# Kernel tuning notes

Hardware: AMD Instinct MI355X
Metric: run time of the kernel (lower is better)

## Reference

```python
import jax, jax.numpy as jnp
import numpy as np

B, TQ, TKV, D, H = 2, 1024, 1024, 1024, 16
HD = D // H
BUCKETS, MAX_REL = 32, 128
SPAN = BUCKETS  # pos_ebd_size


def make_log_bucket_position(rel_pos, bucket_size, max_position):
    sign = jnp.sign(rel_pos)
    mid = bucket_size // 2
    abs_pos = jnp.where((rel_pos < mid) & (rel_pos > -mid), mid - 1, jnp.abs(rel_pos))
    log_pos = jnp.ceil(jnp.log(abs_pos.astype(jnp.float32) / mid)
                       / np.float32(np.log((max_position - 1) / mid)) * (mid - 1)) + mid
    return jnp.where(abs_pos <= mid, rel_pos, (log_pos * sign).astype(rel_pos.dtype))


def setup_inputs():
    key = jax.random.key(0)
    ks = jax.random.split(key, 12)
    s = 0.02
    f32 = jnp.float32
    return {
        "query_states": jax.random.normal(ks[0], (B, TQ, D), f32),
        "key_value_states": jax.random.normal(ks[1], (B, TKV, D), f32),
        "Wq": jax.random.normal(ks[2], (D, D), f32) * s, "bq": jnp.zeros((D,), f32),
        "Wk": jax.random.normal(ks[3], (D, D), f32) * s, "bk": jnp.zeros((D,), f32),
        "Wv": jax.random.normal(ks[4], (D, D), f32) * s, "bv": jnp.zeros((D,), f32),
        "Wo": jax.random.normal(ks[5], (D, D), f32) * s, "bo": jnp.zeros((D,), f32),
        "Wpk": jax.random.normal(ks[6], (D, D), f32) * s, "bpk": jnp.zeros((D,), f32),
        "Wpq": jax.random.normal(ks[7], (D, D), f32) * s, "bpq": jnp.zeros((D,), f32),
        "rel_emb": jax.random.normal(ks[8], (2 * SPAN, D), f32) * s,
        "ln_g": jnp.ones((D,), f32), "ln_b": jnp.zeros((D,), f32),
        "attention_mask": jnp.zeros((B, TKV), jnp.bool_),
    }


def reference(query_states, key_value_states, Wq, bq, Wk, bk, Wv, bv, Wo, bo,
              Wpk, bpk, Wpq, bpq, rel_emb, ln_g, ln_b, attention_mask):
    # projections -> [B,H,T,hd]
    q = (query_states @ Wq.T + bq).reshape(B, TQ, H, HD).transpose(0, 2, 1, 3)
    k = (key_value_states @ Wk.T + bk).reshape(B, TKV, H, HD).transpose(0, 2, 1, 3)
    v = (key_value_states @ Wv.T + bv).reshape(B, TKV, H, HD).transpose(0, 2, 1, 3)
    scale = jnp.sqrt(jnp.float32(HD * 3))  # scale_factor = 1 + c2p + p2c
    scores = jnp.einsum('bhqd,bhkd->bhqk', q, k) / scale

    # layer-normalized relative embeddings [2*SPAN, D]
    mu = rel_emb.mean(-1, keepdims=True)
    var = ((rel_emb - mu) ** 2).mean(-1, keepdims=True)
    re = (rel_emb - mu) * jax.lax.rsqrt(var + 1e-5) * ln_g + ln_b
    pos_k = (re @ Wpk.T + bpk).reshape(2 * SPAN, H, HD).transpose(1, 0, 2)  # [H,2S,hd]
    pos_q = (re @ Wpq.T + bpq).reshape(2 * SPAN, H, HD).transpose(1, 0, 2)

    rel = make_log_bucket_position(jnp.arange(TQ)[:, None] - jnp.arange(TKV)[None, :],
                                   BUCKETS, MAX_REL)                      # [Tq,Tkv]
    c2p_pos = jnp.clip(rel + SPAN, 0, 2 * SPAN - 1)
    p2c_pos = jnp.clip(-rel + SPAN, 0, 2 * SPAN - 1)
    pscale = jnp.sqrt(jnp.float32(HD * 2))

    # c2p: gather along relative-position axis
    c2p = jnp.einsum('bhqd,hpd->bhqp', q, pos_k)                          # [B,H,Tq,2S]
    iq = jnp.arange(TQ)[:, None]
    c2p_g = c2p[:, :, iq, c2p_pos]                                        # [B,H,Tq,Tkv]

    # p2c: gather then transpose (requires Tq == Tkv, as in original torch expand)
    p2c = jnp.einsum('bhkd,hpd->bhkp', k, pos_q)                          # [B,H,Tkv,2S]
    ik = jnp.arange(TKV)[:, None]
    p2c_g = p2c[:, :, ik, p2c_pos].transpose(0, 1, 3, 2)                  # [B,H,Tq,Tkv]

    scores = scores + c2p_g / pscale + p2c_g / pscale
    scores = jnp.where(attention_mask[:, None, None, :], -jnp.inf, scores)
    probs = jax.nn.softmax(scores.astype(jnp.float32), axis=-1).astype(q.dtype)

    ctx = jnp.einsum('bhqk,bhkd->bhqd', probs, v).transpose(0, 2, 1, 3).reshape(B, TQ, D)
    return ctx @ Wo.T + bo
```

## Files before the change

### kernel.cpp

```cpp
#include <hip/hip_runtime.h>
#include <hip/hip_bf16.h>
#include <math.h>

#define B   2
#define TQ  1024
#define TKV 1024
#define D   1024
#define H   16
#define HD  64
#define P   64
#define SPAN 32

#define NEG_INF (-3.0e38f)

typedef __attribute__((ext_vector_type(8))) short bf16x8;
typedef __attribute__((ext_vector_type(4))) float f32x4;
typedef unsigned short ushort_t;

static constexpr size_t RE_OFF   = 0;
static constexpr size_t POSK_OFF = (size_t)64 * 1024;
static constexpr size_t POSQ_OFF = (size_t)128 * 1024;
static constexpr size_t FLOATS_END = (size_t)192 * 1024;
static constexpr size_t SHORT_BASE_BYTES = FLOATS_END * 4;
static constexpr size_t C2P_S  = 0;
static constexpr size_t P2C_S  = (size_t)2 * 1024 * 1024;
static constexpr size_t QH_S   = (size_t)4 * 1024 * 1024;
static constexpr size_t QL_S   = (size_t)6 * 1024 * 1024;
static constexpr size_t KH_S   = (size_t)8 * 1024 * 1024;
static constexpr size_t KL_S   = (size_t)10 * 1024 * 1024;
static constexpr size_t VTH_S  = (size_t)12 * 1024 * 1024;
static constexpr size_t VTL_S  = (size_t)14 * 1024 * 1024;
static constexpr size_t CTXH_S = (size_t)16 * 1024 * 1024;
static constexpr size_t CTXL_S = (size_t)18 * 1024 * 1024;
static constexpr size_t AKVH_S = (size_t)20 * 1024 * 1024;
static constexpr size_t AKVL_S = (size_t)22 * 1024 * 1024;
static constexpr size_t TAB_OFF_BYTES = SHORT_BASE_BYTES + (size_t)24 * 1024 * 1024 * 2;

__device__ __forceinline__ void split2(float x, unsigned short& h, unsigned short& l) {
  unsigned int u = __float_as_uint(x);
  h = (unsigned short)(u >> 16);
  float r = x - __uint_as_float(u & 0xffff0000u);
  unsigned int v = __float_as_uint(r);
  v += 0x7fffu + ((v >> 16) & 1u);
  l = (unsigned short)(v >> 16);
}

__device__ __forceinline__ unsigned short bf16rn(float x) {
  unsigned int v = __float_as_uint(x);
  v += 0x7fffu + ((v >> 16) & 1u);
  return (unsigned short)(v >> 16);
}

__device__ __forceinline__ float bf2f(unsigned short u) {
  return __uint_as_float(((unsigned int)u) << 16);
}

__global__ __launch_bounds__(256) void presplit_kernel(const float* __restrict__ in,
    ushort_t* __restrict__ oh, ushort_t* __restrict__ ol) {
  size_t i = ((size_t)blockIdx.x * 256 + threadIdx.x) * 8;
  float4 a = *(const float4*)&in[i];
  float4 b = *(const float4*)&in[i + 4];
  float xs[8] = {a.x, a.y, a.z, a.w, b.x, b.y, b.z, b.w};
  bf16x8 th, tl;
  #pragma unroll
  for (int j = 0; j < 8; j++) {
    unsigned short hh, ll;
    split2(xs[j], hh, ll);
    th[j] = (short)hh; tl[j] = (short)ll;
  }
  *(bf16x8*)&oh[i] = th;
  *(bf16x8*)&ol[i] = tl;
}

__global__ __launch_bounds__(256) void ln_kernel(const float* __restrict__ x,
    const float* __restrict__ g, const float* __restrict__ bta, float* __restrict__ out) {
  const int row = blockIdx.x;
  const float* xr = x + (size_t)row * D;
  const int tid = threadIdx.x;
  __shared__ float red[4];
  float s = 0.f;
  for (int i = tid; i < D; i += 256) s += xr[i];
  #pragma unroll
  for (int off = 32; off; off >>= 1) s += __shfl_down(s, off);
  if ((tid & 63) == 0) red[tid >> 6] = s;
  __syncthreads();
  float mu = (red[0] + red[1] + red[2] + red[3]) * (1.0f / D);
  __syncthreads();
  float vs = 0.f;
  for (int i = tid; i < D; i += 256) { float dd = xr[i] - mu; vs += dd * dd; }
  #pragma unroll
  for (int off = 32; off; off >>= 1) vs += __shfl_down(vs, off);
  if ((tid & 63) == 0) red[tid >> 6] = vs;
  __syncthreads();
  float var = (red[0] + red[1] + red[2] + red[3]) * (1.0f / D);
  float rs = rsqrtf(var + 1e-5f);
  for (int i = tid; i < D; i += 256)
    out[(size_t)row * D + i] = (xr[i] - mu) * rs * g[i] + bta[i];
}

__global__ void tab_kernel(unsigned char* __restrict__ tab) {
  int i = blockIdx.x * 256 + threadIdx.x;
  if (i >= 2047) return;
  int d = i - 1023;
  int ad = d < 0 ? -d : d;
  int bucket;
  if (ad <= 16) {
    bucket = d;
  } else {
    double x = log((double)ad / 16.0) / log(127.0 / 16.0) * 15.0;
    double xr = floor(x + 0.5);
    double xc = (fabs(x - xr) < 1e-9) ? xr : ceil(x);
    int li = (int)xc + 16;
    bucket = (d > 0) ? li : -li;
  }
  int t = bucket + SPAN;
  t = t < 0 ? 0 : (t > 63 ? 63 : t);
  tab[i] = (unsigned char)t;
}

__global__ __launch_bounds__(256) void gemm_pos(const float* __restrict__ A,
    const float* __restrict__ W0, const float* __restrict__ b0, float* __restrict__ C0,
    const float* __restrict__ W1, const float* __restrict__ b1, float* __restrict__ C1) {
  const float* W = blockIdx.z ? W1 : W0;
  const float* bias = blockIdx.z ? b1 : b0;
  float* C = blockIdx.z ? C1 : C0;

  __shared__ short sAh[64 * 32], sAl[64 * 32], sBh[64 * 32], sBl[64 * 32];
  const int t = threadIdx.x;
  const int bn = blockIdx.x * 64;
  const int wid = t >> 6, lane = t & 63;
  const int wr = wid >> 1, wc = wid & 1;
  const int fr = lane & 15, fo = (lane >> 4) * 8;
  const int srow = t >> 3, scol = (t & 7) * 4;

  f32x4 acc[2][2];
  #pragma unroll
  for (int i = 0; i < 2; i++)
    #pragma unroll
    for (int j = 0; j < 2; j++) acc[i][j] = (f32x4){0.f, 0.f, 0.f, 0.f};

  float4 rA[2], rW[2];
  auto ld = [&](int k0) {
    #pragma unroll
    for (int i = 0; i < 2; i++) {
      rA[i] = *(const float4*)&A[(size_t)(srow + 32 * i) * 1024 + k0 + scol];
      rW[i] = *(const float4*)&W[(size_t)(bn + srow + 32 * i) * 1024 + k0 + scol];
    }
  };
  ld(0);

  for (int k0 = 0; k0 < 1024; k0 += 32) {
    __syncthreads();
    #pragma unroll
    for (int i = 0; i < 2; i++) {
      int row = srow + 32 * i;
      unsigned short h0,h1,h2,h3,l0,l1,l2,l3;
      split2(rA[i].x,h0,l0); split2(rA[i].y,h1,l1); split2(rA[i].z,h2,l2); split2(rA[i].w,h3,l3);
      *(short4*)&sAh[row * 32 + scol] = make_short4((short)h0,(short)h1,(short)h2,(short)h3);
      *(short4*)&sAl[row * 32 + scol] = make_short4((short)l0,(short)l1,(short)l2,(short)l3);
      split2(rW[i].x,h0,l0); split2(rW[i].y,h1,l1); split2(rW[i].z,h2,l2); split2(rW[i].w,h3,l3);
      *(short4*)&sBh[row * 32 + scol] = make_short4((short)h0,(short)h1,(short)h2,(short)h3);
      *(short4*)&sBl[row * 32 + scol] = make_short4((short)l0,(short)l1,(short)l2,(short)l3);
    }
    if (k0 + 32 < 1024) ld(k0 + 32);
    __syncthreads();

    bf16x8 ah[2], al[2], bh[2], bl[2];
    #pragma unroll
    for (int mf = 0; mf < 2; mf++) {
      int r = (wr * 32 + mf * 16 + fr) * 32 + fo;
      ah[mf] = *(const bf16x8*)&sAh[r];
      al[mf] = *(const bf16x8*)&sAl[r];
    }
    #pragma unroll
    for (int nf = 0; nf < 2; nf++) {
      int r = (wc * 32 + nf * 16 + fr) * 32 + fo;
      bh[nf] = *(const bf16x8*)&sBh[r];
      bl[nf] = *(const bf16x8*)&sBl[r];
    }
    #pragma unroll
    for (int mf = 0; mf < 2; mf++)
      #pragma unroll
      for (int nf = 0; nf < 2; nf++) {
        acc[mf][nf] = __builtin_amdgcn_mfma_f32_16x16x32_bf16(ah[mf], bh[nf], acc[mf][nf], 0, 0, 0);
        acc[mf][nf] = __builtin_amdgcn_mfma_f32_16x16x32_bf16(ah[mf], bl[nf], acc[mf][nf], 0, 0, 0);
        acc[mf][nf] = __builtin_amdgcn_mfma_f32_16x16x32_bf16(al[mf], bh[nf], acc[mf][nf], 0, 0, 0);
      }
  }

  #pragma unroll
  for (int mf = 0; mf < 2; mf++) {
    int rbase = wr * 32 + mf * 16 + (lane >> 4) * 4;
    #pragma unroll
    for (int nf = 0; nf < 2; nf++) {
      int col = bn + wc * 32 + nf * 16 + fr;
      float bb = bias[col];
      #pragma unroll
      for (int r = 0; r < 4; r++)
        C[(size_t)(rbase + r) * 1024 + col] = acc[mf][nf][r] + bb;
    }
  }
}

__global__ __launch_bounds__(256) void gemm_split(
    const float* __restrict__ Aq,
    const ushort_t* __restrict__ AKVH, const ushort_t* __restrict__ AKVL,
    const float* __restrict__ W0, const float* __restrict__ W1, const float* __restrict__ W2,
    const float* __restrict__ b0, const float* __restrict__ b1, const float* __restrict__ b2,
    ushort_t* __restrict__ QH_, ushort_t* __restrict__ QL_,
    ushort_t* __restrict__ KH_, ushort_t* __restrict__ KL_,
    ushort_t* __restrict__ VH_, ushort_t* __restrict__ VL_,
    int K) {
  const int z = blockIdx.z;
  const float* W = (z == 0) ? W0 : (z == 1) ? W1 : W2;
  const float* bias = (z == 0) ? b0 : (z == 1) ? b1 : b2;

  const int flat2 = blockIdx.y * 16 + blockIdx.x;
  const int nid = (flat2 & 7) * 32 + (flat2 >> 3);
  const int bn = (nid & 15) * 64;
  const int bm = (nid >> 4) * 128;

  __shared__ short sAhi[128 * 32];
  __shared__ short sAlo[128 * 32];
  __shared__ short sBhi[64 * 32];
  __shared__ short sBlo[64 * 32];

  const int t = threadIdx.x;
  const int wid = t >> 6, lane = t & 63;
  const int wr = wid >> 1, wc = wid & 1;
  const int fr = lane & 15, fo = (lane >> 4) * 8;

  f32x4 acc[4][2];
  #pragma unroll
  for (int i = 0; i < 4; i++)
    #pragma unroll
    for (int j = 0; j < 2; j++)
      acc[i][j] = (f32x4){0.f, 0.f, 0.f, 0.f};

  const int srow = t >> 3;
  const int scol = (t & 7) * 4;
  const int ar = t >> 1;
  const int ac = (t & 1) * 16;

  float4 rA[4], rW[2];
  bf16x8 rAH[2], rAL[2];
  auto ld = [&](int k0) {
    if (z == 0) {
      #pragma unroll
      for (int i = 0; i < 4; i++)
        rA[i] = *(const float4*)&Aq[(size_t)(bm + srow + 32 * i) * K + k0 + scol];
    } else {
      const size_t abase = (size_t)(bm + ar) * K + k0 + ac;
      rAH[0] = *(const bf16x8*)&AKVH[abase];
      rAH[1] = *(const bf16x8*)&AKVH[abase + 8];
      rAL[0] = *(const bf16x8*)&AKVL[abase];
      rAL[1] = *(const bf16x8*)&AKVL[abase + 8];
    }
    #pragma unroll
    for (int i = 0; i < 2; i++)
      rW[i] = *(const float4*)&W[(size_t)(bn + srow + 32 * i) * K + k0 + scol];
  };
  ld(0);

  for (int k0 = 0; k0 < K; k0 += 32) {
    __syncthreads();
    if (z == 0) {
      #pragma unroll
      for (int i = 0; i < 4; i++) {
        int row = srow + 32 * i;
        unsigned short h0, h1, h2, h3, l0, l1, l2, l3;
        split2(rA[i].x, h0, l0); split2(rA[i].y, h1, l1); split2(rA[i].z, h2, l2); split2(rA[i].w, h3, l3);
        *(short4*)&sAhi[row * 32 + scol] = make_short4((short)h0, (short)h1, (short)h2, (short)h3);
        *(short4*)&sAlo[row * 32 + scol] = make_short4((short)l0, (short)l1, (short)l2, (short)l3);
      }
    } else {
      *(bf16x8*)&sAhi[ar * 32 + ac]     = rAH[0];
      *(bf16x8*)&sAhi[ar * 32 + ac + 8] = rAH[1];
      *(bf16x8*)&sAlo[ar * 32 + ac]     = rAL[0];
      *(bf16x8*)&sAlo[ar * 32 + ac + 8] = rAL[1];
    }
    #pragma unroll
    for (int i = 0; i < 2; i++) {
      int row = srow + 32 * i;
      unsigned short h0, h1, h2, h3, l0, l1, l2, l3;
      split2(rW[i].x, h0, l0); split2(rW[i].y, h1, l1); split2(rW[i].z, h2, l2); split2(rW[i].w, h3, l3);
      *(short4*)&sBhi[row * 32 + scol] = make_short4((short)h0, (short)h1, (short)h2, (short)h3);
      *(short4*)&sBlo[row * 32 + scol] = make_short4((short)l0, (short)l1, (short)l2, (short)l3);
    }
    if (k0 + 32 < K) ld(k0 + 32);
    __syncthreads();

    bf16x8 ah[4], al[4], bh[2], bl[2];
    #pragma unroll
    for (int mf = 0; mf < 4; mf++) {
      int r = (wr * 64 + mf * 16 + fr) * 32 + fo;
      ah[mf] = *(const bf16x8*)&sAhi[r];
      al[mf] = *(const bf16x8*)&sAlo[r];
    }
    #pragma unroll
    for (int nf = 0; nf < 2; nf++) {
      int r = (wc * 32 + nf * 16 + fr) * 32 + fo;
      bh[nf] = *(const bf16x8*)&sBhi[r];
      bl[nf] = *(const bf16x8*)&sBlo[r];
    }
    #pragma unroll
    for (int mf = 0; mf < 4; mf++)
      #pragma unroll
      for (int nf = 0; nf < 2; nf++) {
        acc[mf][nf] = __builtin_amdgcn_mfma_f32_16x16x32_bf16(ah[mf], bh[nf], acc[mf][nf], 0, 0, 0);
        acc[mf][nf] = __builtin_amdgcn_mfma_f32_16x16x32_bf16(ah[mf], bl[nf], acc[mf][nf], 0, 0, 0);
        acc[mf][nf] = __builtin_amdgcn_mfma_f32_16x16x32_bf16(al[mf], bh[nf], acc[mf][nf], 0, 0, 0);
      }
  }

  if (z == 2) {
    #pragma unroll
    for (int mf = 0; mf < 4; mf++) {
      int m0 = bm + wr * 64 + mf * 16 + (lane >> 4) * 4;
      int bb2 = m0 >> 10, t0 = m0 & 1023;
      #pragma unroll
      for (int nf = 0; nf < 2; nf++) {
        int col = bn + wc * 32 + nf * 16 + fr;
        int hh = col >> 6, dd = col & 63;
        float bvv = bias[col];
        unsigned short h4[4], l4[4];
        #pragma unroll
        for (int r = 0; r < 4; r++) split2(acc[mf][nf][r] + bvv, h4[r], l4[r]);
        size_t dst = (((size_t)bb2 * 16 + hh) * 64 + dd) * 1024 + t0;
        *(short4*)&VH_[dst] = make_short4((short)h4[0], (short)h4[1], (short)h4[2], (short)h4[3]);
        *(short4*)&VL_[dst] = make_short4((short)l4[0], (short)l4[1], (short)l4[2], (short)l4[3]);
      }
    }
  } else {
    ushort_t* OH = (z == 0) ? QH_ : KH_;
    ushort_t* OL = (z == 0) ? QL_ : KL_;
    #pragma unroll
    for (int mf = 0; mf < 4; mf++) {
      int rbase = bm + wr * 64 + mf * 16 + (lane >> 4) * 4;
      #pragma unroll
      for (int nf = 0; nf < 2; nf++) {
        int col = bn + wc * 32 + nf * 16 + fr;
        float bb = bias[col];
        #pragma unroll
        for (int r = 0; r < 4; r++) {
          unsigned short hh, ll;
          split2(acc[mf][nf][r] + bb, hh, ll);
          OH[(size_t)(rbase + r) * 1024 + col] = hh;
          OL[(size_t)(rbase + r) * 1024 + col] = ll;
        }
      }
    }
  }
}

__global__ __launch_bounds__(256) void gemm_out(
    const ushort_t* __restrict__ AH, const ushort_t* __restrict__ AL,
    const float* __restrict__ W, const float* __restrict__ bias, float* __restrict__ C) {
  __shared__ short sAh[64 * 32], sAl[64 * 32], sBh[64 * 32], sBl[64 * 32];
  const int t = threadIdx.x;
  const int flat2 = blockIdx.y * 16 + blockIdx.x;
  const int nid = (flat2 & 7) * 64 + (flat2 >> 3);
  const int bn = (nid & 15) * 64;
  const int bm = (nid >> 4) * 64;
  const int wid = t >> 6, lane = t & 63;
  const int wr = wid >> 1, wc = wid & 1;
  const int fr = lane & 15, fo = (lane >> 4) * 8;
  const int arow = t >> 2, achk = (t & 3) * 8;
  const int srow = t >> 3, scol = (t & 7) * 4;

  f32x4 acc[2][2];
  #pragma unroll
  for (int i = 0; i < 2; i++)
    #pragma unroll
    for (int j = 0; j < 2; j++) acc[i][j] = (f32x4){0.f, 0.f, 0.f, 0.f};

  bf16x8 rAH, rAL;
  float4 rW[2];
  auto ld = [&](int k0) {
    rAH = *(const bf16x8*)&AH[(size_t)(bm + arow) * 1024 + k0 + achk];
    rAL = *(const bf16x8*)&AL[(size_t)(bm + arow) * 1024 + k0 + achk];
    #pragma unroll
    for (int i = 0; i < 2; i++)
      rW[i] = *(const float4*)&W[(size_t)(bn + srow + 32 * i) * 1024 + k0 + scol];
  };
  ld(0);

  for (int k0 = 0; k0 < 1024; k0 += 32) {
    __syncthreads();
    *(bf16x8*)&sAh[arow * 32 + achk] = rAH;
    *(bf16x8*)&sAl[arow * 32 + achk] = rAL;
    #pragma unroll
    for (int i = 0; i < 2; i++) {
      int row = srow + 32 * i;
      unsigned short h0,h1,h2,h3,l0,l1,l2,l3;
      split2(rW[i].x,h0,l0); split2(rW[i].y,h1,l1); split2(rW[i].z,h2,l2); split2(rW[i].w,h3,l3);
      *(short4*)&sBh[row * 32 + scol] = make_short4((short)h0,(short)h1,(short)h2,(short)h3);
      *(short4*)&sBl[row * 32 + scol] = make_short4((short)l0,(short)l1,(short)l2,(short)l3);
    }
    if (k0 + 32 < 1024) ld(k0 + 32);
    __syncthreads();

    bf16x8 ah[2], al[2], bh[2], bl[2];
    #pragma unroll
    for (int mf = 0; mf < 2; mf++) {
      int r = (wr * 32 + mf * 16 + fr) * 32 + fo;
      ah[mf] = *(const bf16x8*)&sAh[r];
      al[mf] = *(const bf16x8*)&sAl[r];
    }
    #pragma unroll
    for (int nf = 0; nf < 2; nf++) {
      int r = (wc * 32 + nf * 16 + fr) * 32 + fo;
      bh[nf] = *(const bf16x8*)&sBh[r];
      bl[nf] = *(const bf16x8*)&sBl[r];
    }
    #pragma unroll
    for (int mf = 0; mf < 2; mf++)
      #pragma unroll
      for (int nf = 0; nf < 2; nf++) {
        acc[mf][nf] = __builtin_amdgcn_mfma_f32_16x16x32_bf16(ah[mf], bh[nf], acc[mf][nf], 0, 0, 0);
        acc[mf][nf] = __builtin_amdgcn_mfma_f32_16x16x32_bf16(ah[mf], bl[nf], acc[mf][nf], 0, 0, 0);
        acc[mf][nf] = __builtin_amdgcn_mfma_f32_16x16x32_bf16(al[mf], bh[nf], acc[mf][nf], 0, 0, 0);
      }
  }

  #pragma unroll
  for (int mf = 0; mf < 2; mf++) {
    int rbase = bm + wr * 32 + mf * 16 + (lane >> 4) * 4;
    #pragma unroll
    for (int nf = 0; nf < 2; nf++) {
      int col = bn + wc * 32 + nf * 16 + fr;
      float bb = bias[col];
      #pragma unroll
      for (int r = 0; r < 4; r++)
        C[(size_t)(rbase + r) * 1024 + col] = acc[mf][nf][r] + bb;
    }
  }
}

__global__ __launch_bounds__(256) void relproj_kernel(
    const ushort_t* __restrict__ XH0, const ushort_t* __restrict__ XL0,
    const float* __restrict__ P0, ushort_t* __restrict__ O0,
    const ushort_t* __restrict__ XH1, const ushort_t* __restrict__ XL1,
    const float* __restrict__ P1, ushort_t* __restrict__ O1) {
  const int z = blockIdx.z;
  const ushort_t* XH = z ? XH1 : XH0;
  const ushort_t* XL = z ? XL1 : XL0;
  const float* POS = z ? P1 : P0;
  ushort_t* out = z ? O1 : O0;
  const int bh = blockIdx.y, b = bh >> 4, h = bh & 15;
  const int t0 = blockIdx.x * 64;
  __shared__ __align__(16) float sx[64][68];
  __shared__ __align__(16) float sp[64][68];
  const int tid = threadIdx.x;
  for (int i = tid; i < 4096; i += 256) {
    int r = i >> 6, d = i & 63;
    size_t idx = ((size_t)b * TQ + t0 + r) * D + h * HD + d;
    sx[d][r] = bf2f(XH[idx]) + bf2f(XL[idx]);
    sp[d][r] = POS[(size_t)r * D + h * HD + d];
  }
  __syncthreads();
  const int tx = tid & 15, ty = tid >> 4;
  float acc[4][4] = {};
  for (int d = 0; d < 64; d++) {
    float4 a4 = *(const float4*)&sx[d][ty * 4];
    float4 b4 = *(const float4*)&sp[d][tx * 4];
    float av[4] = {a4.x, a4.y, a4.z, a4.w};
    float bv[4] = {b4.x, b4.y, b4.z, b4.w};
    #pragma unroll
    for (int i = 0; i < 4; i++)
      #pragma unroll
      for (int j = 0; j < 4; j++)
        acc[i][j] += av[i] * bv[j];
  }
  const float inv_ps = 0.08838834764831845f;
  #pragma unroll
  for (int i = 0; i < 4; i++)
    #pragma unroll
    for (int j = 0; j < 4; j++)
      out[((size_t)bh * TQ + t0 + ty * 4 + i) * P + tx * 4 + j] = bf16rn(acc[i][j] * inv_ps);
}

__global__ __launch_bounds__(256) void attn_mfma(
    const ushort_t* __restrict__ QHB, const ushort_t* __restrict__ QLB,
    const ushort_t* __restrict__ KH, const ushort_t* __restrict__ KL,
    const ushort_t* __restrict__ VTH, const ushort_t* __restrict__ VTL,
    const ushort_t* __restrict__ c2p, const ushort_t* __restrict__ p2c,
    const unsigned char* __restrict__ mask, const unsigned char* __restrict__ tab,
    ushort_t* __restrict__ CTXH, ushort_t* __restrict__ CTXL) {
  const int flat = blockIdx.y * gridDim.x + blockIdx.x;
  const int nid = (flat & 7) * 64 + (flat >> 3);
  const int bh = nid >> 4, b = bh >> 4, h = bh & 15;
  const int q0 = (nid & 15) * 64;

  const int tid = threadIdx.x;
  const int wid = tid >> 6, lane = tid & 63;
  const int g = lane >> 4, fr = lane & 15;

  __shared__ __align__(16) short sKh[4096], sKl[4096], sVh[4096], sVl[4096];
  __shared__ __align__(16) ushort_t sc2p[64][72];
  __shared__ __align__(16) ushort_t sp2c[64][72];
  __shared__ unsigned char stab[2048];
  __shared__ unsigned char smask[64];

  bf16x8 qh[2], ql[2];
  {
    const int qrow = q0 + wid * 16 + fr;
    const size_t qidx = ((size_t)b * TQ + qrow) * D + h * HD + g * 8;
    #pragma unroll
    for (int ks = 0; ks < 2; ks++) {
      qh[ks] = *(const bf16x8*)&QHB[qidx + ks * 32];
      ql[ks] = *(const bf16x8*)&QLB[qidx + ks * 32];
    }
  }

  const int sr = tid >> 2;
  const int sj0 = tid & 3;
  const int smf = sr >> 4, sfr = sr & 15;
  const int cb = (tid & 3) * 16;
  const int qloc = wid * 16 + fr;

  {
    const ushort_t* cp = c2p + ((size_t)bh * TQ + q0 + sr) * P + cb;
    *(bf16x8*)&sc2p[sr][cb]     = *(const bf16x8*)cp;
    *(bf16x8*)&sc2p[sr][cb + 8] = *(const bf16x8*)(cp + 8);
  }
  for (int i = tid; i < 2047; i += 256) stab[i] = tab[i];
  __syncthreads();
  const float c2p0  = bf2f(sc2p[qloc][0]);
  const float c2p63 = bf2f(sc2p[qloc][63]);

  f32x4 acc[4];
  #pragma unroll
  for (int nf = 0; nf < 4; nf++) acc[nf] = (f32x4){0.f, 0.f, 0.f, 0.f};
  float m_run = NEG_INF, l_run = 0.f;

  const float inv_s = 0.07216878364870323f;

  bf16x8 rKh[2], rKl[2], rVh[2], rVl[2], rP0, rP1;
  unsigned char rmask = 0;

  auto load_tile = [&](int kt) {
    const int k0n = kt * 64;
    const size_t kbase = ((size_t)b * TKV + k0n + sr) * D + h * HD;
    const size_t vbase = ((size_t)bh * HD + sr) * TKV + k0n;
    const ushort_t* pp = p2c + ((size_t)bh * TKV + k0n + sr) * P + cb;
    #pragma unroll
    for (int u = 0; u < 2; u++) {
      int jj = sj0 + u * 4;
      rKh[u] = *(const bf16x8*)(KH + kbase + jj * 8);
      rKl[u] = *(const bf16x8*)(KL + kbase + jj * 8);
      rVh[u] = *(const bf16x8*)(VTH + vbase + jj * 8);
      rVl[u] = *(const bf16x8*)(VTL + vbase + jj * 8);
    }
    rP0 = *(const bf16x8*)pp;
    rP1 = *(const bf16x8*)(pp + 8);
    if (tid < 64) rmask = mask[(size_t)b * TKV + k0n + tid];
  };

  load_tile(0);

  for (int kt = 0; kt < TKV / 64; kt++) {
    const int k0 = kt * 64;
    __syncthreads();
    #pragma unroll
    for (int u = 0; u < 2; u++) {
      int jj = sj0 + u * 4;
      int sub = smf * 8 + (jj >> 2) * 4 + (jj & 3);
      *(bf16x8*)&sKh[sub * 128 + sfr * 8] = rKh[u];
      *(bf16x8*)&sKl[sub * 128 + sfr * 8] = rKl[u];
      *(bf16x8*)&sVh[sub * 128 + sfr * 8] = rVh[u];
      *(bf16x8*)&sVl[sub * 128 + sfr * 8] = rVl[u];
    }
    *(bf16x8*)&sp2c[sr][cb]     = rP0;
    *(bf16x8*)&sp2c[sr][cb + 8] = rP1;
    if (tid < 64) smask[tid] = rmask;
    if (kt + 1 < TKV / 64) load_tile(kt + 1);
    __syncthreads();

    f32x4 st[4];
    #pragma unroll
    for (int mf = 0; mf < 4; mf++) st[mf] = (f32x4){0.f, 0.f, 0.f, 0.f};
    __builtin_amdgcn_s_setprio(1);
    #pragma unroll
    for (int mf = 0; mf < 4; mf++) {
      #pragma unroll
      for (int ks = 0; ks < 2; ks++) {
        bf16x8 kh = *(const bf16x8*)&sKh[(mf * 8 + ks * 4 + g) * 128 + fr * 8];
        bf16x8 kl = *(const bf16x8*)&sKl[(mf * 8 + ks * 4 + g) * 128 + fr * 8];
        st[mf] = __builtin_amdgcn_mfma_f32_16x16x32_bf16(kh, qh[ks], st[mf], 0, 0, 0);
        st[mf] = __builtin_amdgcn_mfma_f32_16x16x32_bf16(kh, ql[ks], st[mf], 0, 0, 0);
        st[mf] = __builtin_amdgcn_mfma_f32_16x16x32_bf16(kl, qh[ks], st[mf], 0, 0, 0);
      }
    }
    __builtin_amdgcn_s_setprio(0);

    const int dtile = q0 - k0;
    float pv[4][4];
    float lmax = NEG_INF;
    if (dtile >= 192 || dtile <= -192) {
      const int C = (dtile >= 192) ? 63 : 0;
      const float cbias = (dtile >= 192) ? c2p63 : c2p0;
      #pragma unroll
      for (int mf = 0; mf < 4; mf++) {
        #pragma unroll
        for (int rr = 0; rr < 4; rr++) {
          int kj = mf * 16 + g * 4 + rr;
          float v = st[mf][rr] * inv_s + (cbias + bf2f(sp2c[kj][C]));
          v = smask[kj] ? NEG_INF : v;
          pv[mf][rr] = v;
          lmax = fmaxf(lmax, v);
        }
      }
    } else {
      const int dq = q0 + qloc - k0 + 1023;
      const ushort_t* c2prow = &sc2p[qloc][0];
      #pragma unroll
      for (int mf = 0; mf < 4; mf++) {
        #pragma unroll
        for (int rr = 0; rr < 4; rr++) {
          int kj = mf * 16 + g * 4 + rr;
          int tbi = stab[dq - kj];
          float v = st[mf][rr] * inv_s + (bf2f(c2prow[tbi]) + bf2f(sp2c[kj][tbi]));
          v = smask[kj] ? NEG_INF : v;
          pv[mf][rr] = v;
          lmax = fmaxf(lmax, v);
        }
      }
    }
    lmax = fmaxf(lmax, __shfl_xor(lmax, 16));
    lmax = fmaxf(lmax, __shfl_xor(lmax, 32));
    if (!__all(lmax <= m_run)) {
      float mnew = fmaxf(m_run, lmax);
      float fac = __expf(m_run - mnew);
      m_run = mnew;
      l_run *= fac;
      float facr[4];
      #pragma unroll
      for (int rr = 0; rr < 4; rr++) facr[rr] = __shfl(fac, g * 4 + rr);
      #pragma unroll
      for (int nf = 0; nf < 4; nf++)
        #pragma unroll
        for (int rr = 0; rr < 4; rr++) acc[nf][rr] *= facr[rr];
    }
    float psum = 0.f;
    #pragma unroll
    for (int mf = 0; mf < 4; mf++)
      #pragma unroll
      for (int rr = 0; rr < 4; rr++) {
        float e = __expf(pv[mf][rr] - m_run);
        pv[mf][rr] = e;
        psum += e;
      }
    psum += __shfl_xor(psum, 16);
    psum += __shfl_xor(psum, 32);
    l_run += psum;

    bf16x8 pa[2];
    #pragma unroll
    for (int ks = 0; ks < 2; ks++) {
      bf16x8 t;
      #pragma unroll
      for (int j = 0; j < 8; j++) {
        int src = ((2 * (g & 1) + (j >> 2)) << 4) | fr;
        float v0 = __shfl(pv[2 * ks][j & 3], src);
        float v1 = __shfl(pv[2 * ks + 1][j & 3], src);
        float pvv = (g >> 1) ? v1 : v0;
        t[j] = (short)bf16rn(pvv);
      }
      pa[ks] = t;
    }

    __builtin_amdgcn_s_setprio(1);
    #pragma unroll
    for (int nf = 0; nf < 4; nf++) {
      #pragma unroll
      for (int ks = 0; ks < 2; ks++) {
        bf16x8 vh = *(const bf16x8*)&sVh[(nf * 8 + ks * 4 + g) * 128 + fr * 8];
        bf16x8 vl = *(const bf16x8*)&sVl[(nf * 8 + ks * 4 + g) * 128 + fr * 8];
        acc[nf] = __builtin_amdgcn_mfma_f32_16x16x32_bf16(pa[ks], vh, acc[nf], 0, 0, 0);
        acc[nf] = __builtin_amdgcn_mfma_f32_16x16x32_bf16(pa[ks], vl, acc[nf], 0, 0, 0);
      }
    }
    __builtin_amdgcn_s_setprio(0);
  }

  float invl[4];
  #pragma unroll
  for (int rr = 0; rr < 4; rr++) invl[rr] = 1.0f / __shfl(l_run, g * 4 + rr);
  #pragma unroll
  for (int nf = 0; nf < 4; nf++) {
    #pragma unroll
    for (int rr = 0; rr < 4; rr++) {
      int qrow = q0 + wid * 16 + g * 4 + rr;
      int dcol = h * HD + nf * 16 + fr;
      size_t idx = ((size_t)b * TQ + qrow) * D + dcol;
      unsigned short hh, ll;
      split2(acc[nf][rr] * invl[rr], hh, ll);
      CTXH[idx] = hh;
      CTXL[idx] = ll;
    }
  }
}

extern "C" void kernel_launch(void* const* d_in, const int* in_sizes, int n_in,
                              void* d_out, int out_size, void* d_ws, size_t ws_size,
                              hipStream_t stream) {
  const float* query = (const float*)d_in[0];
  const float* kv    = (const float*)d_in[1];
  const float* Wq  = (const float*)d_in[2];   const float* bq  = (const float*)d_in[3];
  const float* Wk  = (const float*)d_in[4];   const float* bk  = (const float*)d_in[5];
  const float* Wv  = (const float*)d_in[6];   const float* bv  = (const float*)d_in[7];
  const float* Wo  = (const float*)d_in[8];   const float* bo  = (const float*)d_in[9];
  const float* Wpk = (const float*)d_in[10];  const float* bpk = (const float*)d_in[11];
  const float* Wpq = (const float*)d_in[12];  const float* bpq = (const float*)d_in[13];
  const float* rel_emb = (const float*)d_in[14];
  const float* ln_g = (const float*)d_in[15];
  const float* ln_b = (const float*)d_in[16];
  const unsigned char* amask = (const unsigned char*)d_in[17];

  float* ws = (float*)d_ws;
  float* rebuf   = ws + RE_OFF;
  float* poskbuf = ws + POSK_OFF;
  float* posqbuf = ws + POSQ_OFF;
  ushort_t* sbase = (ushort_t*)((char*)d_ws + SHORT_BASE_BYTES);
  ushort_t* c2pbuf = sbase + C2P_S;
  ushort_t* p2cbuf = sbase + P2C_S;
  ushort_t* QH   = sbase + QH_S;
  ushort_t* QL   = sbase + QL_S;
  ushort_t* KH   = sbase + KH_S;
  ushort_t* KL   = sbase + KL_S;
  ushort_t* VTH  = sbase + VTH_S;
  ushort_t* VTL  = sbase + VTL_S;
  ushort_t* CTXH = sbase + CTXH_S;
  ushort_t* CTXL = sbase + CTXL_S;
  ushort_t* AKVH = sbase + AKVH_S;
  ushort_t* AKVL = sbase + AKVL_S;
  unsigned char* tab = (unsigned char*)d_ws + TAB_OFF_BYTES;

  ln_kernel<<<64, 256, 0, stream>>>(rel_emb, ln_g, ln_b, rebuf);
  tab_kernel<<<8, 256, 0, stream>>>(tab);
  presplit_kernel<<<1024, 256, 0, stream>>>(kv, AKVH, AKVL);
  gemm_pos<<<dim3(16, 1, 2), 256, 0, stream>>>(rebuf, Wpk, bpk, poskbuf, Wpq, bpq, posqbuf);
  gemm_split<<<dim3(16, 16, 3), 256, 0, stream>>>(
      query, AKVH, AKVL,  Wq, Wk, Wv,  bq, bk, bv,
      QH, QL, KH, KL, VTH, VTL, 1024);
  relproj_kernel<<<dim3(16, 32, 2), 256, 0, stream>>>(
      QH, QL, poskbuf, c2pbuf, KH, KL, posqbuf, p2cbuf);
  attn_mfma<<<dim3(16, 32), 256, 0, stream>>>(QH, QL, KH, KL, VTH, VTL,
                                              c2pbuf, p2cbuf, amask, tab, CTXH, CTXL);
  gemm_out<<<dim3(16, 32), 256, 0, stream>>>(CTXH, CTXL, Wo, bo, (float*)d_out);
}
```

Before: 199.4 us.

## Fuse preprocessing kernels, remap GEMM tile order, and move relproj to MFMA

Three small prep kernels (kv bf16 split, rel_emb layernorm, bucket table) are merged into one launch to cut launch overhead. The block-to-tile mapping in gemm_split and gemm_out is changed so that blocks sharing one XCD (flat2&7) cover a compact 2D region for better L2 reuse. The scalar-FMA relative-position projection is replaced by a split-bf16 MFMA kernel (hi/lo three-product emulation) with larger per-block tiles. This keeps near-fp32 accuracy but gives fewer blocks in relproj, and the fused kernel has branch-divergent block roles.

```diff
diff --git a/kernel.cpp b/kernel.cpp
--- a/kernel.cpp
+++ b/kernel.cpp
@@ -55,67 +55,68 @@
   return __uint_as_float(((unsigned int)u) << 16);
 }
 
-__global__ __launch_bounds__(256) void presplit_kernel(const float* __restrict__ in,
-    ushort_t* __restrict__ oh, ushort_t* __restrict__ ol) {
-  size_t i = ((size_t)blockIdx.x * 256 + threadIdx.x) * 8;
-  float4 a = *(const float4*)&in[i];
-  float4 b = *(const float4*)&in[i + 4];
-  float xs[8] = {a.x, a.y, a.z, a.w, b.x, b.y, b.z, b.w};
-  bf16x8 th, tl;
-  #pragma unroll
-  for (int j = 0; j < 8; j++) {
-    unsigned short hh, ll;
-    split2(xs[j], hh, ll);
-    th[j] = (short)hh; tl[j] = (short)ll;
-  }
-  *(bf16x8*)&oh[i] = th;
-  *(bf16x8*)&ol[i] = tl;
-}
-
-__global__ __launch_bounds__(256) void ln_kernel(const float* __restrict__ x,
-    const float* __restrict__ g, const float* __restrict__ bta, float* __restrict__ out) {
-  const int row = blockIdx.x;
-  const float* xr = x + (size_t)row * D;
+__global__ __launch_bounds__(256) void fused_pre(const float* __restrict__ kv,
+    ushort_t* __restrict__ oh, ushort_t* __restrict__ ol,
+    const float* __restrict__ re_in, const float* __restrict__ ln_g,
+    const float* __restrict__ ln_b, float* __restrict__ re_out,
+    unsigned char* __restrict__ tab) {
+  const int bid = blockIdx.x;
   const int tid = threadIdx.x;
-  __shared__ float red[4];
-  float s = 0.f;
-  for (int i = tid; i < D; i += 256) s += xr[i];
-  #pragma unroll
-  for (int off = 32; off; off >>= 1) s += __shfl_down(s, off);
-  if ((tid & 63) == 0) red[tid >> 6] = s;
-  __syncthreads();
-  float mu = (red[0] + red[1] + red[2] + red[3]) * (1.0f / D);
-  __syncthreads();
-  float vs = 0.f;
-  for (int i = tid; i < D; i += 256) { float dd = xr[i] - mu; vs += dd * dd; }
-  #pragma unroll
-  for (int off = 32; off; off >>= 1) vs += __shfl_down(vs, off);
-  if ((tid & 63) == 0) red[tid >> 6] = vs;
-  __syncthreads();
-  float var = (red[0] + red[1] + red[2] + red[3]) * (1.0f / D);
-  float rs = rsqrtf(var + 1e-5f);
-  for (int i = tid; i < D; i += 256)
-    out[(size_t)row * D + i] = (xr[i] - mu) * rs * g[i] + bta[i];
-}
-
-__global__ void tab_kernel(unsigned char* __restrict__ tab) {
-  int i = blockIdx.x * 256 + threadIdx.x;
-  if (i >= 2047) return;
-  int d = i - 1023;
-  int ad = d < 0 ? -d : d;
-  int bucket;
-  if (ad <= 16) {
-    bucket = d;
+  if (bid < 1024) {
+    size_t i = ((size_t)bid * 256 + tid) * 8;
+    float4 a = *(const float4*)&kv[i];
+    float4 b = *(const float4*)&kv[i + 4];
+    float xs[8] = {a.x, a.y, a.z, a.w, b.x, b.y, b.z, b.w};
+    bf16x8 th, tl;
+    #pragma unroll
+    for (int j = 0; j < 8; j++) {
+      unsigned short hh, ll;
+      split2(xs[j], hh, ll);
+      th[j] = (short)hh; tl[j] = (short)ll;
+    }
+    *(bf16x8*)&oh[i] = th;
+    *(bf16x8*)&ol[i] = tl;
+  } else if (bid < 1088) {
+    const int row = bid - 1024;
+    const float* xr = re_in + (size_t)row * D;
+    __shared__ float red[4];
+    float s = 0.f;
+    for (int i = tid; i < D; i += 256) s += xr[i];
+    #pragma unroll
+    for (int off = 32; off; off >>= 1) s += __shfl_down(s, off);
+    if ((tid & 63) == 0) red[tid >> 6] = s;
+    __syncthreads();
+    float mu = (red[0] + red[1] + red[2] + red[3]) * (1.0f / D);
+    __syncthreads();
+    float vs = 0.f;
+    for (int i = tid; i < D; i += 256) { float dd = xr[i] - mu; vs += dd * dd; }
+    #pragma unroll
+    for (int off = 32; off; off >>= 1) vs += __shfl_down(vs, off);
+    if ((tid & 63) == 0) red[tid >> 6] = vs;
+    __syncthreads();
+    float var = (red[0] + red[1] + red[2] + red[3]) * (1.0f / D);
+    float rs = rsqrtf(var + 1e-5f);
+    for (int i = tid; i < D; i += 256)
+      re_out[(size_t)row * D + i] = (xr[i] - mu) * rs * ln_g[i] + ln_b[i];
   } else {
-    double x = log((double)ad / 16.0) / log(127.0 / 16.0) * 15.0;
-    double xr = floor(x + 0.5);
-    double xc = (fabs(x - xr) < 1e-9) ? xr : ceil(x);
-    int li = (int)xc + 16;
-    bucket = (d > 0) ? li : -li;
-  }
-  int t = bucket + SPAN;
-  t = t < 0 ? 0 : (t > 63 ? 63 : t);
-  tab[i] = (unsigned char)t;
+    int i = (bid - 1088) * 256 + tid;
+    if (i >= 2047) return;
+    int d = i - 1023;
+    int ad = d < 0 ? -d : d;
+    int bucket;
+    if (ad <= 16) {
+      bucket = d;
+    } else {
+      double x = log((double)ad / 16.0) / log(127.0 / 16.0) * 15.0;
+      double xr = floor(x + 0.5);
+      double xc = (fabs(x - xr) < 1e-9) ? xr : ceil(x);
+      int li = (int)xc + 16;
+      bucket = (d > 0) ? li : -li;
+    }
+    int t = bucket + SPAN;
+    t = t < 0 ? 0 : (t > 63 ? 63 : t);
+    tab[i] = (unsigned char)t;
+  }
 }
 
 __global__ __launch_bounds__(256) void gemm_pos(const float* __restrict__ A,
@@ -216,9 +217,9 @@
   const float* bias = (z == 0) ? b0 : (z == 1) ? b1 : b2;
 
   const int flat2 = blockIdx.y * 16 + blockIdx.x;
-  const int nid = (flat2 & 7) * 32 + (flat2 >> 3);
-  const int bn = (nid & 15) * 64;
-  const int bm = (nid >> 4) * 128;
+  const int x = flat2 & 7, w = flat2 >> 3;
+  const int bm = ((x >> 1) * 4 + (w >> 3)) * 128;
+  const int bn = ((x & 1) * 8 + (w & 7)) * 64;
 
   __shared__ short sAhi[128 * 32];
   __shared__ short sAlo[128 * 32];
@@ -359,9 +360,9 @@
   __shared__ short sAh[64 * 32], sAl[64 * 32], sBh[64 * 32], sBl[64 * 32];
   const int t = threadIdx.x;
   const int flat2 = blockIdx.y * 16 + blockIdx.x;
-  const int nid = (flat2 & 7) * 64 + (flat2 >> 3);
-  const int bn = (nid & 15) * 64;
-  const int bm = (nid >> 4) * 64;
+  const int x = flat2 & 7, w = flat2 >> 3;
+  const int bm = ((x >> 1) * 8 + (w >> 3)) * 64;
+  const int bn = ((x & 1) * 8 + (w & 7)) * 64;
   const int wid = t >> 6, lane = t & 63;
   const int wr = wid >> 1, wc = wid & 1;
   const int fr = lane & 15, fo = (lane >> 4) * 8;
@@ -437,47 +438,86 @@
   }
 }
 
-__global__ __launch_bounds__(256) void relproj_kernel(
-    const ushort_t* __restrict__ XH0, const ushort_t* __restrict__ XL0,
-    const float* __restrict__ P0, ushort_t* __restrict__ O0,
-    const ushort_t* __restrict__ XH1, const ushort_t* __restrict__ XL1,
-    const float* __restrict__ P1, ushort_t* __restrict__ O1) {
+__global__ __launch_bounds__(256) void relproj_mfma(
+    const ushort_t* __restrict__ QH, const ushort_t* __restrict__ QL,
+    const ushort_t* __restrict__ KH, const ushort_t* __restrict__ KL,
+    const float* __restrict__ POSK, const float* __restrict__ POSQ,
+    ushort_t* __restrict__ O0, ushort_t* __restrict__ O1) {
   const int z = blockIdx.z;
-  const ushort_t* XH = z ? XH1 : XH0;
-  const ushort_t* XL = z ? XL1 : XL0;
-  const float* POS = z ? P1 : P0;
+  const ushort_t* XH = z ? KH : QH;
+  const ushort_t* XL = z ? KL : QL;
+  const float* POS = z ? POSQ : POSK;
   ushort_t* out = z ? O1 : O0;
   const int bh = blockIdx.y, b = bh >> 4, h = bh & 15;
-  const int t0 = blockIdx.x * 64;
-  __shared__ __align__(16) float sx[64][68];
-  __shared__ __align__(16) float sp[64][68];
+  const int t0 = blockIdx.x * 256;
+
   const int tid = threadIdx.x;
-  for (int i = tid; i < 4096; i += 256) {
-    int r = i >> 6, d = i & 63;
-    size_t idx = ((size_t)b * TQ + t0 + r) * D + h * HD + d;
-    sx[d][r] = bf2f(XH[idx]) + bf2f(XL[idx]);
-    sp[d][r] = POS[(size_t)r * D + h * HD + d];
+  const int wid = tid >> 6, lane = tid & 63;
+  const int g = lane >> 4, fr = lane & 15;
+
+  __shared__ __align__(16) short sPh[4096], sPl[4096];
+  {
+    const int sr = tid >> 2;
+    const int cb = (tid & 3) * 16;
+    const float* pp = &POS[(size_t)sr * 1024 + h * HD + cb];
+    #pragma unroll
+    for (int o = 0; o < 16; o += 8) {
+      float4 a = *(const float4*)(pp + o);
+      float4 c = *(const float4*)(pp + o + 4);
+      float xs[8] = {a.x, a.y, a.z, a.w, c.x, c.y, c.z, c.w};
+      bf16x8 th, tl;
+      #pragma unroll
+      for (int j = 0; j < 8; j++) {
+        unsigned short hh, ll;
+        split2(xs[j], hh, ll);
+        th[j] = (short)hh; tl[j] = (short)ll;
+      }
+      int d0 = cb + o;
+      int addr = (((sr >> 4) * 8) + ((d0 >> 5) * 4) + ((d0 >> 3) & 3)) * 128 + (sr & 15) * 8;
+      *(bf16x8*)&sPh[addr] = th;
+      *(bf16x8*)&sPl[addr] = tl;
+    }
   }
   __syncthreads();
-  const int tx = tid & 15, ty = tid >> 4;
-  float acc[4][4] = {};
-  for (int d = 0; d < 64; d++) {
-    float4 a4 = *(const float4*)&sx[d][ty * 4];
-    float4 b4 = *(const float4*)&sp[d][tx * 4];
-    float av[4] = {a4.x, a4.y, a4.z, a4.w};
-    float bv[4] = {b4.x, b4.y, b4.z, b4.w};
-    #pragma unroll
-    for (int i = 0; i < 4; i++)
-      #pragma unroll
-      for (int j = 0; j < 4; j++)
-        acc[i][j] += av[i] * bv[j];
-  }
+
   const float inv_ps = 0.08838834764831845f;
-  #pragma unroll
-  for (int i = 0; i < 4; i++)
-    #pragma unroll
-    for (int j = 0; j < 4; j++)
-      out[((size_t)bh * TQ + t0 + ty * 4 + i) * P + tx * 4 + j] = bf16rn(acc[i][j] * inv_ps);
+  f32x4 acc[4][4];
+  #pragma unroll
+  for (int mf = 0; mf < 4; mf++)
+    #pragma unroll
+    for (int nf = 0; nf < 4; nf++) acc[mf][nf] = (f32x4){0.f, 0.f, 0.f, 0.f};
+
+  #pragma unroll
+  for (int mf = 0; mf < 4; mf++) {
+    const int trow = t0 + wid * 64 + mf * 16 + fr;
+    const size_t xbase = ((size_t)b * TQ + trow) * D + h * HD;
+    #pragma unroll
+    for (int ks = 0; ks < 2; ks++) {
+      bf16x8 ah = *(const bf16x8*)&XH[xbase + ks * 32 + g * 8];
+      bf16x8 al = *(const bf16x8*)&XL[xbase + ks * 32 + g * 8];
+      #pragma unroll
+      for (int nf = 0; nf < 4; nf++) {
+        bf16x8 bhf = *(const bf16x8*)&sPh[(nf * 8 + ks * 4 + g) * 128 + fr * 8];
+        bf16x8 blf = *(const bf16x8*)&sPl[(nf * 8 + ks * 4 + g) * 128 + fr * 8];
+        acc[mf][nf] = __builtin_amdgcn_mfma_f32_16x16x32_bf16(ah, bhf, acc[mf][nf], 0, 0, 0);
+        acc[mf][nf] = __builtin_amdgcn_mfma_f32_16x16x32_bf16(ah, blf, acc[mf][nf], 0, 0, 0);
+        acc[mf][nf] = __builtin_amdgcn_mfma_f32_16x16x32_bf16(al, bhf, acc[mf][nf], 0, 0, 0);
+      }
+    }
+  }
+
+  #pragma unroll
+  for (int mf = 0; mf < 4; mf++) {
+    #pragma unroll
+    for (int nf = 0; nf < 4; nf++) {
+      int p = nf * 16 + fr;
+      #pragma unroll
+      for (int rr = 0; rr < 4; rr++) {
+        int tt = t0 + wid * 64 + mf * 16 + g * 4 + rr;
+        out[((size_t)bh * TQ + tt) * P + p] = bf16rn(acc[mf][nf][rr] * inv_ps);
+      }
+    }
+  }
 }
 
 __global__ __launch_bounds__(256) void attn_mfma(
@@ -737,15 +777,13 @@
   ushort_t* AKVL = sbase + AKVL_S;
   unsigned char* tab = (unsigned char*)d_ws + TAB_OFF_BYTES;
 
-  ln_kernel<<<64, 256, 0, stream>>>(rel_emb, ln_g, ln_b, rebuf);
-  tab_kernel<<<8, 256, 0, stream>>>(tab);
-  presplit_kernel<<<1024, 256, 0, stream>>>(kv, AKVH, AKVL);
+  fused_pre<<<1096, 256, 0, stream>>>(kv, AKVH, AKVL, rel_emb, ln_g, ln_b, rebuf, tab);
   gemm_pos<<<dim3(16, 1, 2), 256, 0, stream>>>(rebuf, Wpk, bpk, poskbuf, Wpq, bpq, posqbuf);
   gemm_split<<<dim3(16, 16, 3), 256, 0, stream>>>(
       query, AKVH, AKVL,  Wq, Wk, Wv,  bq, bk, bv,
       QH, QL, KH, KL, VTH, VTL, 1024);
-  relproj_kernel<<<dim3(16, 32, 2), 256, 0, stream>>>(
-      QH, QL, poskbuf, c2pbuf, KH, KL, posqbuf, p2cbuf);
+  relproj_mfma<<<dim3(4, 32, 2), 256, 0, stream>>>(
+      QH, QL, KH, KL, poskbuf, posqbuf, c2pbuf, p2cbuf);
   attn_mfma<<<dim3(16, 32), 256, 0, stream>>>(QH, QL, KH, KL, VTH, VTL,
                                               c2pbuf, p2cbuf, amask, tab, CTXH, CTXL);
   gemm_out<<<dim3(16, 32), 256, 0, stream>>>(CTXH, CTXL, Wo, bo, (float*)d_out);
```

New measurement: 189.8 us. -4.8%, faster.
